# Optimization experiments

Measured on AMD Instinct MI355X. Metric: run time of the kernel, lower is better.

Reference implementation:

```python
import jax, jax.numpy as jnp
import numpy as np
from jax import lax

SR = 44100  # sample_rate from __init__ default


def _log_scale(v, mn, mx):
    # Faithful to AudioParameter.validate_and_scale with scale='log':
    # clamp, map log(v) to [0,1] over [log(mn), log(mx)], then rescale LINEARLY to [mn, mx].
    v = float(np.clip(float(v), mn, mx))
    log_min = np.log(max(mn, 1e-6))
    log_max = np.log(mx)
    normalized = (np.log(max(v, 1e-6)) - log_min) / (log_max - log_min)
    return normalized * (mx - mn) + mn


def _eq_coeffs(frequency, gain, q, sr=SR):
    # Parameter validation/scaling (frequency, q are 'log' scale; gain is linear clamp)
    f = _log_scale(frequency, 20.0, 20000.0)
    g = float(np.clip(float(gain), -30.0, 30.0))
    Q = _log_scale(q, 0.1, 30.0)
    # torchaudio.functional.equalizer_biquad ('bell' peaking EQ) coefficients
    w0 = 2.0 * np.pi * f / sr
    A = 10.0 ** (g / 40.0)
    alpha = np.sin(w0) / (2.0 * Q)
    b0 = 1.0 + alpha * A
    b1 = -2.0 * np.cos(w0)
    b2 = 1.0 - alpha * A
    a0 = 1.0 + alpha / A
    a1 = b1
    a2 = 1.0 - alpha / A
    return (b0 / a0, b1 / a0, b2 / a0, a1 / a0, a2 / a0)


def _biquad(x, coefs):
    # Direct-form-I second-order IIR along last axis, vectorized over all leading dims.
    b0, b1, b2, a1, a2 = [jnp.asarray(c, x.dtype) for c in coefs]
    shp = x.shape
    xf = x.reshape(-1, shp[-1])  # (N, T)
    z = jnp.zeros((xf.shape[0],), x.dtype)

    def step(carry, xn):
        x1, x2, y1, y2 = carry
        yn = b0 * xn + b1 * x1 + b2 * x2 - a1 * y1 - a2 * y2
        return (xn, x1, yn, y1), yn

    _, ys = lax.scan(step, (z, z, z, z), xf.T)  # ys: (T, N)
    return ys.T.reshape(shp)


def setup_inputs() -> dict:
    key = jax.random.key(0)
    audio = jax.random.normal(key, (32, 2, 441000), dtype=jnp.float32)  # 10s stereo, batch 32
    return {"audio": audio, "frequency": 2000, "gain": 6, "q": 1}


def reference(audio, frequency, gain, q):
    # filter_type='bell' (default) -> torchaudio equalizer_biquad path
    coefs = _eq_coeffs(frequency, gain, q)
    return _biquad(audio, coefs)
```

## Files before the change

kernel.cpp:

```cpp
#include <hip/hip_runtime.h>
#include <math.h>

#ifndef M_PI
#define M_PI 3.14159265358979323846
#endif

#define T_LEN      441000
#define L          16
#define BLOCK      256
#define WARM_LANES 16
#define SEG_OUT    ((BLOCK - WARM_LANES) * L)
#define NSEG       ((T_LEN + SEG_OUT - 1) / SEG_OUT)


__device__ __forceinline__ double log_scale(double v, double mn, double mx) {
    v = fmin(fmax(v, mn), mx);
    double lmin = log(fmax(mn, 1e-6));
    double lmax = log(mx);
    double nrm = (log(fmax(v, 1e-6)) - lmin) / (lmax - lmin);
    return nrm * (mx - mn) + mn;
}

__global__ void eq_setup_kernel(const int* __restrict__ f_in,
                                const int* __restrict__ g_in,
                                const int* __restrict__ q_in,
                                float* __restrict__ ws) {
    double f = log_scale((double)f_in[0], 20.0, 20000.0);
    double g = fmin(fmax((double)g_in[0], -30.0), 30.0);
    double Q = log_scale((double)q_in[0], 0.1, 30.0);
    double w0 = 2.0 * M_PI * f / 44100.0;
    double A  = pow(10.0, g / 40.0);
    double al = sin(w0) / (2.0 * Q);
    double ca = cos(w0);
    double b0 = 1.0 + al * A;
    double b1 = -2.0 * ca;
    double b2 = 1.0 - al * A;
    double a0 = 1.0 + al / A;
    double B0 = b0 / a0, B1 = b1 / a0, B2 = b2 / a0;
    double A1 = b1 / a0, A2 = (1.0 - al / A) / a0;
    ws[0] = (float)B0; ws[1] = (float)B1; ws[2] = (float)B2;
    ws[3] = (float)A1; ws[4] = (float)A2;

    double p11 = -A1, p12 = -A2, p21 = 1.0, p22 = 0.0;
    for (int i = 0; i < 4; ++i) {
        double s11 = p11 * p11 + p12 * p21;
        double s12 = p11 * p12 + p12 * p22;
        double s21 = p21 * p11 + p22 * p21;
        double s22 = p21 * p12 + p22 * p22;
        p11 = s11; p12 = s12; p21 = s21; p22 = s22;
    }
    for (int j = 0; j < 7; ++j) {
        ws[5 + 4 * j + 0] = (float)p11;
        ws[5 + 4 * j + 1] = (float)p12;
        ws[5 + 4 * j + 2] = (float)p21;
        ws[5 + 4 * j + 3] = (float)p22;
        double s11 = p11 * p11 + p12 * p21;
        double s12 = p11 * p12 + p12 * p22;
        double s21 = p21 * p11 + p22 * p21;
        double s22 = p21 * p12 + p22 * p22;
        p11 = s11; p12 = s12; p21 = s21; p22 = s22;
    }
}

__global__ __launch_bounds__(BLOCK, 4) void eq_main_kernel(
        const float* __restrict__ x,
        const float* __restrict__ ws,
        float* __restrict__ y) {
    const int tid  = threadIdx.x;
    const int lane = tid & 63;
    const int wv   = tid >> 6;
    const int ch   = blockIdx.y;

    const float b0 = ws[0], b1 = ws[1], b2 = ws[2], a1 = ws[3], a2 = ws[4];

    const float* __restrict__ xc = x + (size_t)ch * T_LEN;
    float*       __restrict__ yc = y + (size_t)ch * T_LEN;

    const int w0   = blockIdx.x * SEG_OUT - WARM_LANES * L;
    const int base = w0 + tid * L;

    float xv[L], xm1, xm2;
    if (base >= 2 && base + L <= T_LEN) {
        const float4 v0 = *reinterpret_cast<const float4*>(xc + base + 0);
        const float4 v1 = *reinterpret_cast<const float4*>(xc + base + 4);
        const float4 v2 = *reinterpret_cast<const float4*>(xc + base + 8);
        const float4 v3 = *reinterpret_cast<const float4*>(xc + base + 12);
        xv[0]=v0.x; xv[1]=v0.y; xv[2]=v0.z; xv[3]=v0.w;
        xv[4]=v1.x; xv[5]=v1.y; xv[6]=v1.z; xv[7]=v1.w;
        xv[8]=v2.x; xv[9]=v2.y; xv[10]=v2.z; xv[11]=v2.w;
        xv[12]=v3.x; xv[13]=v3.y; xv[14]=v3.z; xv[15]=v3.w;
        xm1 = xc[base - 1];
        xm2 = xc[base - 2];
    } else {
#pragma unroll
        for (int k = 0; k < L; ++k) {
            const int idx = base + k;
            xv[k] = (idx >= 0 && idx < T_LEN) ? xc[idx] : 0.f;
        }
        xm1 = (base - 1 >= 0 && base - 1 < T_LEN) ? xc[base - 1] : 0.f;
        xm2 = (base - 2 >= 0 && base - 2 < T_LEN) ? xc[base - 2] : 0.f;
    }

    float t[L];
    t[0] = fmaf(b0, xv[0], fmaf(b1, xm1, b2 * xm2));
    t[1] = fmaf(b0, xv[1], fmaf(b1, xv[0], b2 * xm1));
#pragma unroll
    for (int k = 2; k < L; ++k)
        t[k] = fmaf(b0, xv[k], fmaf(b1, xv[k - 1], b2 * xv[k - 2]));

    float c0 = 0.f, c1 = 0.f;
#pragma unroll
    for (int k = 0; k < L; ++k) {
        const float yn = fmaf(-a1, c0, fmaf(-a2, c1, t[k]));
        c1 = c0; c0 = yn;
    }
    const float l0 = c0, l1 = c1;

#pragma unroll
    for (int j = 0; j < 6; ++j) {
        const float m11 = ws[5 + 4 * j + 0], m12 = ws[5 + 4 * j + 1];
        const float m21 = ws[5 + 4 * j + 2], m22 = ws[5 + 4 * j + 3];
        const float d0 = __shfl_up(c0, 1u << j);
        const float d1 = __shfl_up(c1, 1u << j);
        if (lane >= (1 << j)) {
            c0 = fmaf(m11, d0, fmaf(m12, d1, c0));
            c1 = fmaf(m21, d0, fmaf(m22, d1, c1));
        }
    }

    __shared__ float wsum[BLOCK / 64][2];
    if (lane == 63) { wsum[wv][0] = c0; wsum[wv][1] = c1; }
    __syncthreads();
    const float A11 = ws[5 + 24 + 0], A12 = ws[5 + 24 + 1];
    const float A21 = ws[5 + 24 + 2], A22 = ws[5 + 24 + 3];
    float g0 = 0.f, g1 = 0.f;
    for (int w = 0; w < wv; ++w) {
        const float n0 = fmaf(A11, g0, fmaf(A12, g1, wsum[w][0]));
        const float n1 = fmaf(A21, g0, fmaf(A22, g1, wsum[w][1]));
        g0 = n0; g1 = n1;
    }

    c0 = l0; c1 = l1;
    if (lane == 0) {
        const float m11 = ws[5], m12 = ws[6], m21 = ws[7], m22 = ws[8];
        c0 = fmaf(m11, g0, fmaf(m12, g1, l0));
        c1 = fmaf(m21, g0, fmaf(m22, g1, l1));
    }
#pragma unroll
    for (int j = 0; j < 6; ++j) {
        const float m11 = ws[5 + 4 * j + 0], m12 = ws[5 + 4 * j + 1];
        const float m21 = ws[5 + 4 * j + 2], m22 = ws[5 + 4 * j + 3];
        const float d0 = __shfl_up(c0, 1u << j);
        const float d1 = __shfl_up(c1, 1u << j);
        if (lane >= (1 << j)) {
            c0 = fmaf(m11, d0, fmaf(m12, d1, c0));
            c1 = fmaf(m21, d0, fmaf(m22, d1, c1));
        }
    }
    float s0 = __shfl_up(c0, 1);
    float s1 = __shfl_up(c1, 1);
    if (lane == 0) { s0 = g0; s1 = g1; }

    float yv[L];
    float p0 = s0, p1 = s1;
#pragma unroll
    for (int k = 0; k < L; ++k) {
        const float yn = fmaf(-a1, p0, fmaf(-a2, p1, t[k]));
        p1 = p0; p0 = yn;
        yv[k] = yn;
    }

    if (tid >= WARM_LANES && base < T_LEN) {
        if (base + L <= T_LEN) {
            *reinterpret_cast<float4*>(yc + base + 0)  = make_float4(yv[0], yv[1], yv[2], yv[3]);
            *reinterpret_cast<float4*>(yc + base + 4)  = make_float4(yv[4], yv[5], yv[6], yv[7]);
            *reinterpret_cast<float4*>(yc + base + 8)  = make_float4(yv[8], yv[9], yv[10], yv[11]);
            *reinterpret_cast<float4*>(yc + base + 12) = make_float4(yv[12], yv[13], yv[14], yv[15]);
        } else {
#pragma unroll
            for (int k = 0; k < L; ++k)
                if (base + k < T_LEN) yc[base + k] = yv[k];
        }
    }
}

extern "C" void kernel_launch(void* const* d_in, const int* in_sizes, int n_in,
                              void* d_out, int out_size, void* d_ws, size_t ws_size,
                              hipStream_t stream) {
    const float* x = (const float*)d_in[0];
    const int*   f = (const int*)d_in[1];
    const int*   g = (const int*)d_in[2];
    const int*   q = (const int*)d_in[3];
    float*       y  = (float*)d_out;
    float*       ws = (float*)d_ws;

    eq_setup_kernel<<<1, 1, 0, stream>>>(f, g, q, ws);

    const int nch = in_sizes[0] / T_LEN;
    dim3 grid(NSEG, nch);
    eq_main_kernel<<<grid, dim3(BLOCK), 0, stream>>>(x, ws, y);
}
```

Before: 212.4 us.

## Make each wavefront an independent segment, dropping block-level scan and second pass

Each 64-lane wavefront now handles its own segment with 8 warm-up lanes and 32 samples per lane. This removes the shared-memory cross-wave combine, the __syncthreads and the second shuffle scan. The FIR terms are recomputed on the fly instead of being kept in a t[] array, which cuts register use, and launch bounds are raised to allow higher occupancy. The cost is a larger fraction of redundant warm-up work (8 of 64 lanes) and reliance on the truncated filter history from 256 samples of warm-up being accurate enough.

```diff
diff --git a/kernel.cpp b/kernel.cpp
--- a/kernel.cpp
+++ b/kernel.cpp
@@ -5,12 +5,13 @@
 #define M_PI 3.14159265358979323846
 #endif
 
-#define T_LEN      441000
-#define L          16
-#define BLOCK      256
-#define WARM_LANES 16
-#define SEG_OUT    ((BLOCK - WARM_LANES) * L)
-#define NSEG       ((T_LEN + SEG_OUT - 1) / SEG_OUT)
+#define T_LEN  441000
+#define L      32
+#define WARM   8
+#define SEG_W  ((64 - WARM) * L)
+#define WPC    ((T_LEN + SEG_W - 1) / SEG_W)
+#define BLOCK  256
+#define BLK_X  ((WPC + 3) / 4)
 
 
 __device__ __forceinline__ double log_scale(double v, double mn, double mx) {
@@ -42,14 +43,14 @@
     ws[3] = (float)A1; ws[4] = (float)A2;
 
     double p11 = -A1, p12 = -A2, p21 = 1.0, p22 = 0.0;
-    for (int i = 0; i < 4; ++i) {
+    for (int i = 0; i < 5; ++i) {
         double s11 = p11 * p11 + p12 * p21;
         double s12 = p11 * p12 + p12 * p22;
         double s21 = p21 * p11 + p22 * p21;
         double s22 = p21 * p12 + p22 * p22;
         p11 = s11; p12 = s12; p21 = s21; p22 = s22;
     }
-    for (int j = 0; j < 7; ++j) {
+    for (int j = 0; j < 6; ++j) {
         ws[5 + 4 * j + 0] = (float)p11;
         ws[5 + 4 * j + 1] = (float)p12;
         ws[5 + 4 * j + 2] = (float)p21;
@@ -62,13 +63,15 @@
     }
 }
 
-__global__ __launch_bounds__(BLOCK, 4) void eq_main_kernel(
+__global__ __launch_bounds__(BLOCK, 8) void eq_main_kernel(
         const float* __restrict__ x,
         const float* __restrict__ ws,
         float* __restrict__ y) {
     const int tid  = threadIdx.x;
     const int lane = tid & 63;
     const int wv   = tid >> 6;
+    const int wave = blockIdx.x * (BLOCK / 64) + wv;
+    if (wave * SEG_W >= T_LEN) return;
     const int ch   = blockIdx.y;
 
     const float b0 = ws[0], b1 = ws[1], b2 = ws[2], a1 = ws[3], a2 = ws[4];
@@ -76,21 +79,18 @@
     const float* __restrict__ xc = x + (size_t)ch * T_LEN;
     float*       __restrict__ yc = y + (size_t)ch * T_LEN;
 
-    const int w0   = blockIdx.x * SEG_OUT - WARM_LANES * L;
-    const int base = w0 + tid * L;
+    const int base = wave * SEG_W - WARM * L + lane * L;
 
     float xv[L], xm1, xm2;
-    if (base >= 2 && base + L <= T_LEN) {
-        const float4 v0 = *reinterpret_cast<const float4*>(xc + base + 0);
-        const float4 v1 = *reinterpret_cast<const float4*>(xc + base + 4);
-        const float4 v2 = *reinterpret_cast<const float4*>(xc + base + 8);
-        const float4 v3 = *reinterpret_cast<const float4*>(xc + base + 12);
-        xv[0]=v0.x; xv[1]=v0.y; xv[2]=v0.z; xv[3]=v0.w;
-        xv[4]=v1.x; xv[5]=v1.y; xv[6]=v1.z; xv[7]=v1.w;
-        xv[8]=v2.x; xv[9]=v2.y; xv[10]=v2.z; xv[11]=v2.w;
-        xv[12]=v3.x; xv[13]=v3.y; xv[14]=v3.z; xv[15]=v3.w;
-        xm1 = xc[base - 1];
-        xm2 = xc[base - 2];
+    if (base >= 4 && base + L <= T_LEN) {
+        const float4 vm = *reinterpret_cast<const float4*>(xc + base - 4);
+        xm2 = vm.z; xm1 = vm.w;
+#pragma unroll
+        for (int q = 0; q < L / 4; ++q) {
+            const float4 v = *reinterpret_cast<const float4*>(xc + base + 4 * q);
+            xv[4 * q + 0] = v.x; xv[4 * q + 1] = v.y;
+            xv[4 * q + 2] = v.z; xv[4 * q + 3] = v.w;
+        }
     } else {
 #pragma unroll
         for (int k = 0; k < L; ++k) {
@@ -101,20 +101,18 @@
         xm2 = (base - 2 >= 0 && base - 2 < T_LEN) ? xc[base - 2] : 0.f;
     }
 
-    float t[L];
-    t[0] = fmaf(b0, xv[0], fmaf(b1, xm1, b2 * xm2));
-    t[1] = fmaf(b0, xv[1], fmaf(b1, xv[0], b2 * xm1));
+    float c0 = 0.f, c1 = 0.f;
+    {
+        float xk1 = xm1, xk2 = xm2;
 #pragma unroll
-    for (int k = 2; k < L; ++k)
-        t[k] = fmaf(b0, xv[k], fmaf(b1, xv[k - 1], b2 * xv[k - 2]));
-
-    float c0 = 0.f, c1 = 0.f;
-#pragma unroll
-    for (int k = 0; k < L; ++k) {
-        const float yn = fmaf(-a1, c0, fmaf(-a2, c1, t[k]));
-        c1 = c0; c0 = yn;
+        for (int k = 0; k < L; ++k) {
+            const float xk = xv[k];
+            const float t  = fmaf(b0, xk, fmaf(b1, xk1, b2 * xk2));
+            const float yn = fmaf(-a1, c0, fmaf(-a2, c1, t));
+            c1 = c0; c0 = yn;
+            xk2 = xk1; xk1 = xk;
+        }
     }
-    const float l0 = c0, l1 = c1;
 
 #pragma unroll
     for (int j = 0; j < 6; ++j) {
@@ -128,58 +126,39 @@
         }
     }
 
-    __shared__ float wsum[BLOCK / 64][2];
-    if (lane == 63) { wsum[wv][0] = c0; wsum[wv][1] = c1; }
-    __syncthreads();
-    const float A11 = ws[5 + 24 + 0], A12 = ws[5 + 24 + 1];
-    const float A21 = ws[5 + 24 + 2], A22 = ws[5 + 24 + 3];
-    float g0 = 0.f, g1 = 0.f;
-    for (int w = 0; w < wv; ++w) {
-        const float n0 = fmaf(A11, g0, fmaf(A12, g1, wsum[w][0]));
-        const float n1 = fmaf(A21, g0, fmaf(A22, g1, wsum[w][1]));
-        g0 = n0; g1 = n1;
-    }
-
-    c0 = l0; c1 = l1;
-    if (lane == 0) {
-        const float m11 = ws[5], m12 = ws[6], m21 = ws[7], m22 = ws[8];
-        c0 = fmaf(m11, g0, fmaf(m12, g1, l0));
-        c1 = fmaf(m21, g0, fmaf(m22, g1, l1));
-    }
-#pragma unroll
-    for (int j = 0; j < 6; ++j) {
-        const float m11 = ws[5 + 4 * j + 0], m12 = ws[5 + 4 * j + 1];
-        const float m21 = ws[5 + 4 * j + 2], m22 = ws[5 + 4 * j + 3];
-        const float d0 = __shfl_up(c0, 1u << j);
-        const float d1 = __shfl_up(c1, 1u << j);
-        if (lane >= (1 << j)) {
-            c0 = fmaf(m11, d0, fmaf(m12, d1, c0));
-            c1 = fmaf(m21, d0, fmaf(m22, d1, c1));
-        }
-    }
     float s0 = __shfl_up(c0, 1);
     float s1 = __shfl_up(c1, 1);
-    if (lane == 0) { s0 = g0; s1 = g1; }
+    if (lane == 0) { s0 = 0.f; s1 = 0.f; }
 
-    float yv[L];
-    float p0 = s0, p1 = s1;
+    if (lane >= WARM && base < T_LEN) {
+        float p0 = s0, p1 = s1;
+        float xk1 = xm1, xk2 = xm2;
+        if (base + L <= T_LEN) {
 #pragma unroll
-    for (int k = 0; k < L; ++k) {
-        const float yn = fmaf(-a1, p0, fmaf(-a2, p1, t[k]));
-        p1 = p0; p0 = yn;
-        yv[k] = yn;
-    }
-
-    if (tid >= WARM_LANES && base < T_LEN) {
-        if (base + L <= T_LEN) {
-            *reinterpret_cast<float4*>(yc + base + 0)  = make_float4(yv[0], yv[1], yv[2], yv[3]);
-            *reinterpret_cast<float4*>(yc + base + 4)  = make_float4(yv[4], yv[5], yv[6], yv[7]);
-            *reinterpret_cast<float4*>(yc + base + 8)  = make_float4(yv[8], yv[9], yv[10], yv[11]);
-            *reinterpret_cast<float4*>(yc + base + 12) = make_float4(yv[12], yv[13], yv[14], yv[15]);
+            for (int q = 0; q < L / 4; ++q) {
+                float ov[4];
+#pragma unroll
+                for (int r = 0; r < 4; ++r) {
+                    const float xk = xv[4 * q + r];
+                    const float t  = fmaf(b0, xk, fmaf(b1, xk1, b2 * xk2));
+                    const float yn = fmaf(-a1, p0, fmaf(-a2, p1, t));
+                    p1 = p0; p0 = yn;
+                    xk2 = xk1; xk1 = xk;
+                    ov[r] = yn;
+                }
+                *reinterpret_cast<float4*>(yc + base + 4 * q) =
+                    make_float4(ov[0], ov[1], ov[2], ov[3]);
+            }
         } else {
 #pragma unroll
-            for (int k = 0; k < L; ++k)
-                if (base + k < T_LEN) yc[base + k] = yv[k];
+            for (int k = 0; k < L; ++k) {
+                const float xk = xv[k];
+                const float t  = fmaf(b0, xk, fmaf(b1, xk1, b2 * xk2));
+                const float yn = fmaf(-a1, p0, fmaf(-a2, p1, t));
+                p1 = p0; p0 = yn;
+                xk2 = xk1; xk1 = xk;
+                if (base + k < T_LEN) yc[base + k] = yn;
+            }
         }
     }
 }
@@ -197,6 +176,6 @@
     eq_setup_kernel<<<1, 1, 0, stream>>>(f, g, q, ws);
 
     const int nch = in_sizes[0] / T_LEN;
-    dim3 grid(NSEG, nch);
+    dim3 grid(BLK_X, nch);
     eq_main_kernel<<<grid, dim3(BLOCK), 0, stream>>>(x, ws, y);
 }
```

Result: slower. 229.7 us (+8.1%).
